# Optimization experiments

Hardware: AMD Instinct MI355X
Metric: run time of the kernel (lower is better)

Reference implementation:

```python
import jax, jax.numpy as jnp
import numpy as np

GROUP_SIZE = 32


def dequantize_int4(weight, scales_and_zeros, group_size=GROUP_SIZE):
    """weight: [N, K] int codes in [0,16); scales_and_zeros: [K//gs, N, 2].
    tinygemm convention: w = (q - 8) * scale + zero, groups along K."""
    N, K = weight.shape
    G = K // group_size
    q = weight.astype(scales_and_zeros.dtype).reshape(N, G, group_size)
    scales = scales_and_zeros[:, :, 0].T[:, :, None]  # [N, G, 1]
    zeros = scales_and_zeros[:, :, 1].T[:, :, None]   # [N, G, 1]
    w = (q - 8.0) * scales + zeros
    return w.reshape(N, K)


def setup_inputs() -> dict:
    key = jax.random.key(0)
    k1, k2, k3, k4 = jax.random.split(key, 4)
    M, K, N = 8192, 4096, 12288
    inp = {}
    inp["input"] = jax.random.normal(k1, (M, K), dtype=jnp.float32)
    inp["weight"] = jax.random.randint(k2, (N, K), 0, 16, dtype=jnp.int32)
    # scales small/positive, zeros zero-centered (column 0 = scale, column 1 = zero)
    scales = jax.random.uniform(k3, (K // GROUP_SIZE, N), dtype=jnp.float32) * 0.02 + 1e-3
    zeros = jax.random.normal(k4, (K // GROUP_SIZE, N), dtype=jnp.float32) * 0.05
    inp["scales_and_zeros"] = jnp.stack([scales, zeros], axis=-1)
    inp["bias"] = jax.random.normal(jax.random.fold_in(key, 5), (N,), dtype=jnp.float32)
    return inp


def reference(input, weight, scales_and_zeros, bias):
    # Faithful math of INT4Linear.forward: the tinygemm ops perform a GEMM of
    # input [M,K] against the dequantized int4 weight [N,K] (groupwise
    # scale/zero along K), then add bias. Layout conversions are identity math.
    w_dq = dequantize_int4(weight, scales_and_zeros)  # [N, K]
    y = jnp.einsum("mk,nk->mn", input, w_dq)          # [M, N]
    return y + bias
```

## Files before the change

kernel.cpp:

```cpp
#include <hip/hip_runtime.h>
#include <hip/hip_bf16.h>
#include <cstdint>
#include <cstddef>

#define MM 8192
#define KK 4096
#define NN 12288

typedef __bf16 bf16x8 __attribute__((ext_vector_type(8)));
typedef float  f32x4  __attribute__((ext_vector_type(4)));

__device__ __forceinline__ unsigned short f2bf(float f) {
    union { float f; unsigned int u; } v; v.f = f;
    unsigned int r = v.u + 0x7fffu + ((v.u >> 16) & 1u);
    return (unsigned short)(r >> 16);
}

__device__ __forceinline__ void gload_lds16(const void* g, void* l) {
    __builtin_amdgcn_global_load_lds(
        (__attribute__((address_space(1))) void*)g,
        (__attribute__((address_space(3))) void*)l,
        16, 0, 0);
}

#define FENCE() asm volatile("" ::: "memory")
#define LGKM0() asm volatile("s_waitcnt lgkmcnt(0)" ::: "memory")
#define BARF()  do { FENCE(); __builtin_amdgcn_s_barrier(); FENCE(); } while (0)

__global__ __launch_bounds__(256) void cvt_a_kernel(
    const float* __restrict__ in, unsigned short* __restrict__ out)
{
    size_t i = (size_t)blockIdx.x * 256 + threadIdx.x;
    const float4* p = (const float4*)in;
    float4 x = p[2 * i], y = p[2 * i + 1];
    union { unsigned short h[8]; uint4 v; } u;
    u.h[0] = f2bf(x.x); u.h[1] = f2bf(x.y); u.h[2] = f2bf(x.z); u.h[3] = f2bf(x.w);
    u.h[4] = f2bf(y.x); u.h[5] = f2bf(y.y); u.h[6] = f2bf(y.z); u.h[7] = f2bf(y.w);
    ((uint4*)out)[i] = u.v;
}

__global__ __launch_bounds__(256) void dq_w_kernel(
    const int* __restrict__ w, const float* __restrict__ snz,
    unsigned short* __restrict__ out)
{
    size_t t = (size_t)blockIdx.x * 256 + threadIdx.x;
    int kc = (int)(t & (KK / 8 - 1));
    int n  = (int)(t >> 9);
    int g  = kc >> 2;
    float2 sz = ((const float2*)snz)[(size_t)g * NN + n];
    const int4* wp = (const int4*)w;
    int4 q0 = wp[2 * t], q1 = wp[2 * t + 1];
    union { unsigned short h[8]; uint4 v; } u;
    u.h[0] = f2bf((float)(q0.x - 8) * sz.x + sz.y);
    u.h[1] = f2bf((float)(q0.y - 8) * sz.x + sz.y);
    u.h[2] = f2bf((float)(q0.z - 8) * sz.x + sz.y);
    u.h[3] = f2bf((float)(q0.w - 8) * sz.x + sz.y);
    u.h[4] = f2bf((float)(q1.x - 8) * sz.x + sz.y);
    u.h[5] = f2bf((float)(q1.y - 8) * sz.x + sz.y);
    u.h[6] = f2bf((float)(q1.z - 8) * sz.x + sz.y);
    u.h[7] = f2bf((float)(q1.w - 8) * sz.x + sz.y);
    ((uint4*)out)[t] = u.v;
}

#define BM 256
#define BN 256
#define BK 64
#define TT (KK / BK)

__global__ __launch_bounds__(512, 2) void gemm256_kernel(
    const unsigned short* __restrict__ A,
    const unsigned short* __restrict__ Bw,
    const float* __restrict__ bias,
    float* __restrict__ C)
{
    __shared__ char lds[163840];

    const int tid  = threadIdx.x;
    const int lane = tid & 63;
    const int wave = tid >> 6;
    const int wm   = wave >> 2;
    const int wn   = wave & 3;

    const int NTN = NN / BN;
    const int nwg = (MM / BM) * NTN;
    const int cpx = nwg >> 3;
    int wg = ((int)blockIdx.x & 7) * cpx + ((int)blockIdx.x >> 3);
    const int tm = wg / NTN;
    const int tn = wg - tm * NTN;

    f32x4 acc[8][4] = {};

    const int lrow = lane >> 3;
    const int lc   = (lane & 7) ^ lrow;
    const unsigned short* aSrc = A  + (size_t)(tm * BM + wave * 8 + lrow) * KK + lc * 8;
    const unsigned short* bSrc = Bw + (size_t)(tn * BN + wave * 8 + lrow) * KK + lc * 8;
    const int wblk = wave * 1024;

#define STAGE(srcBase, rowsOff, kOff, ldsPtr) do {                                          \
        gload_lds16((srcBase) + (size_t)(rowsOff) * KK + (kOff), (ldsPtr) + wblk);          \
        gload_lds16((srcBase) + (size_t)((rowsOff) + 64) * KK + (kOff), (ldsPtr) + 8192 + wblk); \
    } while (0)

    const int r7  = lane & 7;
    const int l15 = lane & 15;
    const int c0  = (((lane >> 4)    ) ^ r7) * 16;
    const int c1  = (((lane >> 4) + 4) ^ r7) * 16;
    const int aoff = (wm * 128 + l15) * 128;
    const int boff = (wn * 64  + l15) * 128;

    STAGE(aSrc, 0,   0, lds + 0);
    STAGE(aSrc, 128, 0, lds + 16384);
    STAGE(bSrc, 0,   0, lds + 65536);
    STAGE(bSrc, 128, 0, lds + 65536 + 16384);
    STAGE(aSrc, 0,   BK, lds + 32768);
    STAGE(aSrc, 128, BK, lds + 32768 + 16384);
    STAGE(bSrc, 0,   BK, lds + 65536 + 32768);
    STAGE(bSrc, 128, BK, lds + 65536 + 32768 + 16384);
    asm volatile("s_waitcnt vmcnt(8)" ::: "memory");
    BARF();

    int bRead = 0;
    for (int t = 0; t < TT; ++t) {
        const char* Ab = lds + ((t & 1) << 15);
        const char* Bb = lds + 65536 + (bRead << 15);
        int bs = bRead + 2; if (bs >= 3) bs -= 3;
        char* Bst = lds + 65536 + (bs << 15);
        char* Ast = lds + ((t & 1) << 15);
        const bool pf = (t + 2 < TT);
        const int kpf = (t + 2) * BK;

        bf16x8 a0[8];
#pragma unroll
        for (int mf = 0; mf < 8; ++mf)
            a0[mf] = *(const bf16x8*)(Ab + aoff + mf * 2048 + c0);
        bf16x8 p0b0 = *(const bf16x8*)(Bb + boff + 0 * 2048 + c0);
        bf16x8 p0b1 = *(const bf16x8*)(Bb + boff + 1 * 2048 + c0);
        if (pf) STAGE(bSrc, 0, kpf, Bst);
        BARF(); LGKM0();
        __builtin_amdgcn_s_setprio(1);
#pragma unroll
        for (int mf = 0; mf < 8; ++mf) {
            acc[mf][0] = __builtin_amdgcn_mfma_f32_16x16x32_bf16(a0[mf], p0b0, acc[mf][0], 0, 0, 0);
            acc[mf][1] = __builtin_amdgcn_mfma_f32_16x16x32_bf16(a0[mf], p0b1, acc[mf][1], 0, 0, 0);
        }
        __builtin_amdgcn_s_setprio(0);
        BARF();

        bf16x8 a1[8];
#pragma unroll
        for (int mf = 0; mf < 8; ++mf)
            a1[mf] = *(const bf16x8*)(Ab + aoff + mf * 2048 + c1);
        bf16x8 p1b2 = *(const bf16x8*)(Bb + boff + 2 * 2048 + c0);
        bf16x8 p1b3 = *(const bf16x8*)(Bb + boff + 3 * 2048 + c0);
        if (pf) STAGE(bSrc, 128, kpf, Bst + 16384);
        BARF(); LGKM0();
        __builtin_amdgcn_s_setprio(1);
#pragma unroll
        for (int mf = 0; mf < 8; ++mf) {
            acc[mf][2] = __builtin_amdgcn_mfma_f32_16x16x32_bf16(a0[mf], p1b2, acc[mf][2], 0, 0, 0);
            acc[mf][3] = __builtin_amdgcn_mfma_f32_16x16x32_bf16(a0[mf], p1b3, acc[mf][3], 0, 0, 0);
        }
        __builtin_amdgcn_s_setprio(0);
        BARF();

        bf16x8 p2b0 = *(const bf16x8*)(Bb + boff + 0 * 2048 + c1);
        bf16x8 p2b1 = *(const bf16x8*)(Bb + boff + 1 * 2048 + c1);
        if (pf) STAGE(aSrc, 0, kpf, Ast);
        BARF(); LGKM0();
        __builtin_amdgcn_s_setprio(1);
#pragma unroll
        for (int mf = 0; mf < 8; ++mf) {
            acc[mf][0] = __builtin_amdgcn_mfma_f32_16x16x32_bf16(a1[mf], p2b0, acc[mf][0], 0, 0, 0);
            acc[mf][1] = __builtin_amdgcn_mfma_f32_16x16x32_bf16(a1[mf], p2b1, acc[mf][1], 0, 0, 0);
        }
        __builtin_amdgcn_s_setprio(0);
        BARF();

        bf16x8 p3b2 = *(const bf16x8*)(Bb + boff + 2 * 2048 + c1);
        bf16x8 p3b3 = *(const bf16x8*)(Bb + boff + 3 * 2048 + c1);
        if (pf) STAGE(aSrc, 128, kpf, Ast + 16384);
        BARF(); LGKM0();
        __builtin_amdgcn_s_setprio(1);
#pragma unroll
        for (int mf = 0; mf < 8; ++mf) {
            acc[mf][2] = __builtin_amdgcn_mfma_f32_16x16x32_bf16(a1[mf], p3b2, acc[mf][2], 0, 0, 0);
            acc[mf][3] = __builtin_amdgcn_mfma_f32_16x16x32_bf16(a1[mf], p3b3, acc[mf][3], 0, 0, 0);
        }
        __builtin_amdgcn_s_setprio(0);
        if (t < TT - 1) {
            if (pf) { asm volatile("s_waitcnt vmcnt(8)" ::: "memory"); }
            else    { asm volatile("s_waitcnt vmcnt(0)" ::: "memory"); }
            BARF();
        }
        bRead = bRead + 1; if (bRead >= 3) bRead -= 3;
    }
#undef STAGE

    const int crow = tm * BM + wm * 128 + (lane >> 4) * 4;
    const int ccol = tn * BN + wn * 64 + l15;
    float bv[4];
#pragma unroll
    for (int nf = 0; nf < 4; ++nf) bv[nf] = bias[ccol + nf * 16];
#pragma unroll
    for (int mf = 0; mf < 8; ++mf)
#pragma unroll
        for (int nf = 0; nf < 4; ++nf)
#pragma unroll
            for (int j = 0; j < 4; ++j)
                C[(size_t)(crow + mf * 16 + j) * NN + ccol + nf * 16] =
                    acc[mf][nf][j] + bv[nf];
}

__global__ __launch_bounds__(256) void gemm_fused_kernel(
    const float* __restrict__ Af,
    const int* __restrict__ Wq,
    const float* __restrict__ snz,
    const float* __restrict__ bias,
    float* __restrict__ C)
{
    __shared__ alignas(16) unsigned short As[128 * 64];
    __shared__ alignas(16) unsigned short Bs[128 * 64];

    const int tid  = threadIdx.x;
    const int lane = tid & 63;
    const int wave = tid >> 6;

    const int NTN = NN / 128;
    const int nwg = (MM / 128) * NTN;
    const int cpx = nwg >> 3;
    int wg = ((int)blockIdx.x & 7) * cpx + ((int)blockIdx.x >> 3);
    const int tm = wg / NTN;
    const int tn = wg - tm * NTN;

    const int wm = wave >> 1, wn = wave & 1;

    f32x4 acc[4][4] = {};

    const int r7  = lane & 7;
    const int pc0 = (((lane >> 4)    ) ^ r7) * 16;
    const int pc1 = (((lane >> 4) + 4) ^ r7) * 16;
    const int arow = wm * 64 + (lane & 15);
    const int brow = wn * 64 + (lane & 15);
    const char* AsR = (const char*)As;
    const char* BsR = (const char*)Bs;

    const int frow = tid >> 1;
    const int fh   = tid & 1;
    const int frx  = frow & 7;

    for (int k0 = 0; k0 < KK; k0 += 64) {
        {
            const float* ap = Af + (size_t)(tm * 128 + frow) * KK + k0 + fh * 32;
#pragma unroll
            for (int c = 0; c < 4; ++c) {
                float4 x = ((const float4*)ap)[2 * c];
                float4 y = ((const float4*)ap)[2 * c + 1];
                union { unsigned short h[8]; uint4 v; } u;
                u.h[0] = f2bf(x.x); u.h[1] = f2bf(x.y); u.h[2] = f2bf(x.z); u.h[3] = f2bf(x.w);
                u.h[4] = f2bf(y.x); u.h[5] = f2bf(y.y); u.h[6] = f2bf(y.z); u.h[7] = f2bf(y.w);
                int lc2 = fh * 4 + c;
                *(uint4*)&As[frow * 64 + ((lc2 ^ frx) * 8)] = u.v;
            }
        }
        {
            const int nrow = tn * 128 + frow;
            const int* wp = Wq + (size_t)nrow * KK + k0 + fh * 32;
            float2 sz = ((const float2*)snz)[(size_t)((k0 >> 5) + fh) * NN + nrow];
#pragma unroll
            for (int c = 0; c < 4; ++c) {
                int4 q0 = ((const int4*)wp)[2 * c];
                int4 q1 = ((const int4*)wp)[2 * c + 1];
                union { unsigned short h[8]; uint4 v; } u;
                u.h[0] = f2bf((float)(q0.x - 8) * sz.x + sz.y);
                u.h[1] = f2bf((float)(q0.y - 8) * sz.x + sz.y);
                u.h[2] = f2bf((float)(q0.z - 8) * sz.x + sz.y);
                u.h[3] = f2bf((float)(q0.w - 8) * sz.x + sz.y);
                u.h[4] = f2bf((float)(q1.x - 8) * sz.x + sz.y);
                u.h[5] = f2bf((float)(q1.y - 8) * sz.x + sz.y);
                u.h[6] = f2bf((float)(q1.z - 8) * sz.x + sz.y);
                u.h[7] = f2bf((float)(q1.w - 8) * sz.x + sz.y);
                int lc2 = fh * 4 + c;
                *(uint4*)&Bs[frow * 64 + ((lc2 ^ frx) * 8)] = u.v;
            }
        }
        __syncthreads();
        {
            bf16x8 af[4], bfr[4];
#pragma unroll
            for (int x = 0; x < 4; ++x) {
                af[x]  = *(const bf16x8*)(AsR + (arow + x * 16) * 128 + pc0);
                bfr[x] = *(const bf16x8*)(BsR + (brow + x * 16) * 128 + pc0);
            }
#pragma unroll
            for (int mi = 0; mi < 4; ++mi)
#pragma unroll
                for (int ni = 0; ni < 4; ++ni)
                    acc[mi][ni] = __builtin_amdgcn_mfma_f32_16x16x32_bf16(
                        af[mi], bfr[ni], acc[mi][ni], 0, 0, 0);
        }
        {
            bf16x8 af[4], bfr[4];
#pragma unroll
            for (int x = 0; x < 4; ++x) {
                af[x]  = *(const bf16x8*)(AsR + (arow + x * 16) * 128 + pc1);
                bfr[x] = *(const bf16x8*)(BsR + (brow + x * 16) * 128 + pc1);
            }
#pragma unroll
            for (int mi = 0; mi < 4; ++mi)
#pragma unroll
                for (int ni = 0; ni < 4; ++ni)
                    acc[mi][ni] = __builtin_amdgcn_mfma_f32_16x16x32_bf16(
                        af[mi], bfr[ni], acc[mi][ni], 0, 0, 0);
        }
        __syncthreads();
    }

    const int crow = tm * 128 + wm * 64 + (lane >> 4) * 4;
    const int ccol = tn * 128 + wn * 64 + (lane & 15);
    float bv[4];
#pragma unroll
    for (int ni = 0; ni < 4; ++ni) bv[ni] = bias[ccol + ni * 16];
#pragma unroll
    for (int mi = 0; mi < 4; ++mi)
#pragma unroll
        for (int ni = 0; ni < 4; ++ni)
#pragma unroll
            for (int j = 0; j < 4; ++j)
                C[(size_t)(crow + mi * 16 + j) * NN + ccol + ni * 16] =
                    acc[mi][ni][j] + bv[ni];
}

extern "C" void kernel_launch(void* const* d_in, const int* in_sizes, int n_in,
                              void* d_out, int out_size, void* d_ws, size_t ws_size,
                              hipStream_t stream)
{
    const float* inA  = (const float*)d_in[0];
    const int*   Wq   = (const int*)d_in[1];
    const float* snz  = (const float*)d_in[2];
    const float* bias = (const float*)d_in[3];
    float* out = (float*)d_out;

    const size_t needA = (size_t)MM * KK * 2;
    const size_t needW = (size_t)NN * KK * 2;

    if (ws_size >= needA + needW) {
        unsigned short* Abf = (unsigned short*)d_ws;
        unsigned short* Wbf = (unsigned short*)((char*)d_ws + needA);
        cvt_a_kernel<<<(MM * KK / 8) / 256, 256, 0, stream>>>(inA, Abf);
        dq_w_kernel<<<(NN * KK / 8) / 256, 256, 0, stream>>>(Wq, snz, Wbf);
        gemm256_kernel<<<(MM / BM) * (NN / BN), 512, 0, stream>>>(Abf, Wbf, bias, out);
    } else {
        gemm_fused_kernel<<<(MM / 128) * (NN / 128), 256, 0, stream>>>(
            inA, Wq, snz, bias, out);
    }
}
```

Measured before the change: 817.7 us.

## Software-pipeline LDS fragment reads across MFMA phases, cut barriers per tile

Restructures the GEMM main loop so LDS fragment loads for the next phase, and the next tile's first A fragments, are issued before the current MFMA batches run, using ping-pong A register arrays and a loop unrolled by two. Barriers per K-tile drop from four to two and the explicit lgkmcnt(0) waits are removed, leaving the compiler to insert LDS waits. The goal is to hide LDS latency and barrier stalls behind matrix work. The cost is more live vector registers, which may lower occupancy or cause spills, and a change in how global-to-LDS loads are ordered against reads (vmcnt(4)) that could introduce a race.

```diff
diff --git a/kernel.cpp b/kernel.cpp
--- a/kernel.cpp
+++ b/kernel.cpp
@@ -24,7 +24,6 @@
 }
 
 #define FENCE() asm volatile("" ::: "memory")
-#define LGKM0() asm volatile("s_waitcnt lgkmcnt(0)" ::: "memory")
 #define BARF()  do { FENCE(); __builtin_amdgcn_s_barrier(); FENCE(); } while (0)
 
 __global__ __launch_bounds__(256) void cvt_a_kernel(
@@ -119,81 +118,91 @@
     asm volatile("s_waitcnt vmcnt(8)" ::: "memory");
     BARF();
 
-    int bRead = 0;
-    for (int t = 0; t < TT; ++t) {
-        const char* Ab = lds + ((t & 1) << 15);
-        const char* Bb = lds + 65536 + (bRead << 15);
-        int bs = bRead + 2; if (bs >= 3) bs -= 3;
-        char* Bst = lds + 65536 + (bs << 15);
-        char* Ast = lds + ((t & 1) << 15);
-        const bool pf = (t + 2 < TT);
-        const int kpf = (t + 2) * BK;
-
-        bf16x8 a0[8];
-#pragma unroll
-        for (int mf = 0; mf < 8; ++mf)
-            a0[mf] = *(const bf16x8*)(Ab + aoff + mf * 2048 + c0);
-        bf16x8 p0b0 = *(const bf16x8*)(Bb + boff + 0 * 2048 + c0);
-        bf16x8 p0b1 = *(const bf16x8*)(Bb + boff + 1 * 2048 + c0);
-        if (pf) STAGE(bSrc, 0, kpf, Bst);
-        BARF(); LGKM0();
-        __builtin_amdgcn_s_setprio(1);
-#pragma unroll
-        for (int mf = 0; mf < 8; ++mf) {
-            acc[mf][0] = __builtin_amdgcn_mfma_f32_16x16x32_bf16(a0[mf], p0b0, acc[mf][0], 0, 0, 0);
-            acc[mf][1] = __builtin_amdgcn_mfma_f32_16x16x32_bf16(a0[mf], p0b1, acc[mf][1], 0, 0, 0);
-        }
-        __builtin_amdgcn_s_setprio(0);
-        BARF();
-
-        bf16x8 a1[8];
-#pragma unroll
-        for (int mf = 0; mf < 8; ++mf)
-            a1[mf] = *(const bf16x8*)(Ab + aoff + mf * 2048 + c1);
-        bf16x8 p1b2 = *(const bf16x8*)(Bb + boff + 2 * 2048 + c0);
-        bf16x8 p1b3 = *(const bf16x8*)(Bb + boff + 3 * 2048 + c0);
-        if (pf) STAGE(bSrc, 128, kpf, Bst + 16384);
-        BARF(); LGKM0();
-        __builtin_amdgcn_s_setprio(1);
-#pragma unroll
-        for (int mf = 0; mf < 8; ++mf) {
-            acc[mf][2] = __builtin_amdgcn_mfma_f32_16x16x32_bf16(a0[mf], p1b2, acc[mf][2], 0, 0, 0);
-            acc[mf][3] = __builtin_amdgcn_mfma_f32_16x16x32_bf16(a0[mf], p1b3, acc[mf][3], 0, 0, 0);
-        }
-        __builtin_amdgcn_s_setprio(0);
-        BARF();
-
-        bf16x8 p2b0 = *(const bf16x8*)(Bb + boff + 0 * 2048 + c1);
-        bf16x8 p2b1 = *(const bf16x8*)(Bb + boff + 1 * 2048 + c1);
-        if (pf) STAGE(aSrc, 0, kpf, Ast);
-        BARF(); LGKM0();
-        __builtin_amdgcn_s_setprio(1);
-#pragma unroll
-        for (int mf = 0; mf < 8; ++mf) {
-            acc[mf][0] = __builtin_amdgcn_mfma_f32_16x16x32_bf16(a1[mf], p2b0, acc[mf][0], 0, 0, 0);
-            acc[mf][1] = __builtin_amdgcn_mfma_f32_16x16x32_bf16(a1[mf], p2b1, acc[mf][1], 0, 0, 0);
-        }
-        __builtin_amdgcn_s_setprio(0);
-        BARF();
-
-        bf16x8 p3b2 = *(const bf16x8*)(Bb + boff + 2 * 2048 + c1);
-        bf16x8 p3b3 = *(const bf16x8*)(Bb + boff + 3 * 2048 + c1);
-        if (pf) STAGE(aSrc, 128, kpf, Ast + 16384);
-        BARF(); LGKM0();
-        __builtin_amdgcn_s_setprio(1);
-#pragma unroll
-        for (int mf = 0; mf < 8; ++mf) {
-            acc[mf][2] = __builtin_amdgcn_mfma_f32_16x16x32_bf16(a1[mf], p3b2, acc[mf][2], 0, 0, 0);
-            acc[mf][3] = __builtin_amdgcn_mfma_f32_16x16x32_bf16(a1[mf], p3b3, acc[mf][3], 0, 0, 0);
-        }
-        __builtin_amdgcn_s_setprio(0);
-        if (t < TT - 1) {
-            if (pf) { asm volatile("s_waitcnt vmcnt(8)" ::: "memory"); }
-            else    { asm volatile("s_waitcnt vmcnt(0)" ::: "memory"); }
-            BARF();
-        }
-        bRead = bRead + 1; if (bRead >= 3) bRead -= 3;
+    bf16x8 aA[8], aB[8], a1[8];
+#pragma unroll
+    for (int mf = 0; mf < 8; ++mf)
+        aA[mf] = *(const bf16x8*)(lds + aoff + mf * 2048 + c0);
+
+#define MFMA8(AARR, BREG, NF)                                                     \
+    _Pragma("unroll")                                                             \
+    for (int mf = 0; mf < 8; ++mf)                                                \
+        acc[mf][NF] = __builtin_amdgcn_mfma_f32_16x16x32_bf16(                    \
+            AARR[mf], BREG, acc[mf][NF], 0, 0, 0);
+
+#define TILE(T, BRD, AC, AN) do {                                                 \
+    const char* Ab = lds + (((T) & 1) << 15);                                     \
+    const char* Bb = lds + 65536 + ((BRD) << 15);                                 \
+    int bs_ = (BRD) + 2; if (bs_ >= 3) bs_ -= 3;                                  \
+    char* Bst = lds + 65536 + (bs_ << 15);                                        \
+    char* Ast = lds + (((T) & 1) << 15);                                          \
+    const char* An = lds + (((((T) + 1)) & 1) << 15);                             \
+    const bool pf2 = (T) + 2 < TT;                                                \
+    const bool pf1 = (T) + 1 < TT;                                                \
+    const int kpf = ((T) + 2) * BK;                                               \
+        \
+    bf16x8 b00 = *(const bf16x8*)(Bb + boff + 0 * 2048 + c0);                     \
+    bf16x8 b01 = *(const bf16x8*)(Bb + boff + 1 * 2048 + c0);                     \
+    a1[0] = *(const bf16x8*)(Ab + aoff + 0 * 2048 + c1);                          \
+    a1[1] = *(const bf16x8*)(Ab + aoff + 1 * 2048 + c1);                          \
+    a1[2] = *(const bf16x8*)(Ab + aoff + 2 * 2048 + c1);                          \
+    a1[3] = *(const bf16x8*)(Ab + aoff + 3 * 2048 + c1);                          \
+    if (pf2) STAGE(bSrc, 0, kpf, Bst);                                            \
+    __builtin_amdgcn_s_setprio(1);                                                \
+    MFMA8(AC, b00, 0); MFMA8(AC, b01, 1);                                         \
+    __builtin_amdgcn_s_setprio(0);                                                \
+         \
+    a1[4] = *(const bf16x8*)(Ab + aoff + 4 * 2048 + c1);                          \
+    a1[5] = *(const bf16x8*)(Ab + aoff + 5 * 2048 + c1);                          \
+    a1[6] = *(const bf16x8*)(Ab + aoff + 6 * 2048 + c1);                          \
+    a1[7] = *(const bf16x8*)(Ab + aoff + 7 * 2048 + c1);                          \
+    bf16x8 b02 = *(const bf16x8*)(Bb + boff + 2 * 2048 + c0);                     \
+    bf16x8 b03 = *(const bf16x8*)(Bb + boff + 3 * 2048 + c0);                     \
+    if (pf2) STAGE(bSrc, 128, kpf, Bst + 16384);                                  \
+    __builtin_amdgcn_s_setprio(1);                                                \
+    MFMA8(AC, b02, 2); MFMA8(AC, b03, 3);                                         \
+    __builtin_amdgcn_s_setprio(0);                                                \
+    if (pf2) { asm volatile("s_waitcnt vmcnt(4)" ::: "memory"); }                 \
+    else     { asm volatile("s_waitcnt vmcnt(0)" ::: "memory"); }                 \
+    BARF();                                                                       \
+        \
+    bf16x8 b10 = *(const bf16x8*)(Bb + boff + 0 * 2048 + c1);                     \
+    bf16x8 b11 = *(const bf16x8*)(Bb + boff + 1 * 2048 + c1);                     \
+    if (pf1) {                                                                    \
+        AN[0] = *(const bf16x8*)(An + aoff + 0 * 2048 + c0);                      \
+        AN[1] = *(const bf16x8*)(An + aoff + 1 * 2048 + c0);                      \
+        AN[2] = *(const bf16x8*)(An + aoff + 2 * 2048 + c0);                      \
+        AN[3] = *(const bf16x8*)(An + aoff + 3 * 2048 + c0);                      \
+    }                                                                             \
+    if (pf2) STAGE(aSrc, 0, kpf, Ast);                                            \
+    __builtin_amdgcn_s_setprio(1);                                                \
+    MFMA8(a1, b10, 0); MFMA8(a1, b11, 1);                                         \
+    __builtin_amdgcn_s_setprio(0);                                                \
+                  \
+    bf16x8 b12 = *(const bf16x8*)(Bb + boff + 2 * 2048 + c1);                     \
+    bf16x8 b13 = *(const bf16x8*)(Bb + boff + 3 * 2048 + c1);                     \
+    if (pf1) {                                                                    \
+        AN[4] = *(const bf16x8*)(An + aoff + 4 * 2048 + c0);                      \
+        AN[5] = *(const bf16x8*)(An + aoff + 5 * 2048 + c0);                      \
+        AN[6] = *(const bf16x8*)(An + aoff + 6 * 2048 + c0);                      \
+        AN[7] = *(const bf16x8*)(An + aoff + 7 * 2048 + c0);                      \
+    }                                                                             \
+    if (pf2) STAGE(aSrc, 128, kpf, Ast + 16384);                                  \
+    __builtin_amdgcn_s_setprio(1);                                                \
+    MFMA8(a1, b12, 2); MFMA8(a1, b13, 3);                                         \
+    __builtin_amdgcn_s_setprio(0);                                                \
+    BARF();                                                                       \
+} while (0)
+
+    int bR = 0;
+#pragma unroll 1
+    for (int t2 = 0; t2 < TT; t2 += 2) {
+        int bR1 = bR + 1; if (bR1 >= 3) bR1 -= 3;
+        TILE(t2,     bR,  aA, aB);
+        TILE(t2 + 1, bR1, aB, aA);
+        bR = bR1 + 1; if (bR >= 3) bR -= 3;
     }
+#undef TILE
+#undef MFMA8
 #undef STAGE
 
     const int crow = tm * BM + wm * 128 + (lane >> 4) * 4;
```

Measured after the change: 2.383 ms. +191.4%, slower.
